# Performance work log

Hardware: AMD Instinct MI355X
Metric: run time of the kernel (lower is better)

Reference implementation:

```python
import jax, jax.numpy as jnp
import numpy as np

NUM_HEADS = 16
HEAD_DIM = 64  # hidden_size (1024) // num_heads


def setup_inputs() -> dict:
    key = jax.random.key(0)
    ks = jax.random.split(key, 8)
    B, S, H = 8, 1024, 1024
    scale = 1.0 / np.sqrt(H)
    return {
        "hidden_states": jax.random.normal(ks[0], (B, S, H), dtype=jnp.float32),
        "attention_mask": jnp.zeros((B, 1, 1, S), dtype=jnp.float32),
        "Wq": jax.random.normal(ks[1], (H, H), dtype=jnp.float32) * scale,
        "bq": jnp.zeros((H,), dtype=jnp.float32),
        "Wk": jax.random.normal(ks[2], (H, H), dtype=jnp.float32) * scale,
        "bk": jnp.zeros((H,), dtype=jnp.float32),
        "Wv": jax.random.normal(ks[3], (H, H), dtype=jnp.float32) * scale,
        "bv": jnp.zeros((H,), dtype=jnp.float32),
    }


def _split_heads(x):
    # [B, S, H] -> [B, nh, S, hd]
    B, S, H = x.shape
    return x.reshape(B, S, NUM_HEADS, HEAD_DIM).transpose(0, 2, 1, 3)


def reference(hidden_states, attention_mask, Wq, bq, Wk, bk, Wv, bv):
    # Q/K/V projections (Keras Dense: y = x @ W + b)
    q = _split_heads(hidden_states @ Wq + bq)  # [B, nh, S, hd]
    k = _split_heads(hidden_states @ Wk + bk)
    v = _split_heads(hidden_states @ Wv + bv)

    # Full QK^T score matrix, scaled, plus additive mask (faithful to source)
    scores = jnp.einsum("bhqd,bhkd->bhqk", q, k) / jnp.sqrt(
        jnp.asarray(HEAD_DIM, dtype=q.dtype)
    )
    scores = scores + attention_mask
    probs = jax.nn.softmax(scores, axis=-1)  # [B, nh, Sq, Sk]

    # Weighted sum of values, merge heads back
    ctx = jnp.einsum("bhqk,bhkd->bhqd", probs, v)
    B, _, S, _ = ctx.shape
    ctx = ctx.transpose(0, 2, 1, 3).reshape(B, S, NUM_HEADS * HEAD_DIM)
    return ctx
```

## Files before the change

### kernel.cpp

```cpp
#include <hip/hip_runtime.h>
#include <hip/hip_bf16.h>


typedef float f4 __attribute__((ext_vector_type(4)));
typedef short s8 __attribute__((ext_vector_type(8)));
typedef short s4 __attribute__((ext_vector_type(4)));

#define NB   8
#define SS   1024
#define HH   1024

#define OFF_XB  0u
#define OFF_WT  16777216u
#define OFF_Q   23068672u
#define OFF_K   39845888u
#define OFF_VT  56623104u

static __device__ __forceinline__ unsigned short f2bf(float x){
    unsigned int u = __float_as_uint(x);
    unsigned int r = (u + 0x7fffu + ((u >> 16) & 1u)) >> 16;
    return (unsigned short)r;
}

__global__ void cvt_x_kernel(const float* __restrict__ in, unsigned short* __restrict__ out){
    int i = blockIdx.x * 256 + threadIdx.x;
    f4 a = ((const f4*)in)[2*i];
    f4 b = ((const f4*)in)[2*i+1];
    s8 r;
    #pragma unroll
    for (int j=0;j<4;j++) r[j]   = (short)f2bf(a[j]);
    #pragma unroll
    for (int j=0;j<4;j++) r[4+j] = (short)f2bf(b[j]);
    ((s8*)out)[i] = r;
}

__global__ void cvt_w_kernel(const float* __restrict__ Wq, const float* __restrict__ Wk,
                             const float* __restrict__ Wv, unsigned short* __restrict__ Wt){
    int t = blockIdx.x;
    int which = t >> 8; t &= 255;
    int k0 = (t >> 4) << 6;
    int n0 = (t & 15) << 6;
    const float* W = which==0 ? Wq : (which==1 ? Wk : Wv);
    __shared__ float Ls[64][65];
    int tid = threadIdx.x;
    #pragma unroll
    for (int i=0;i<4;i++){
        int u = tid + i*256;
        int r = u >> 4, ch = u & 15;
        f4 v = *(const f4*)&W[(size_t)(k0 + r)*HH + n0 + ch*4];
        Ls[r][ch*4+0]=v[0]; Ls[r][ch*4+1]=v[1]; Ls[r][ch*4+2]=v[2]; Ls[r][ch*4+3]=v[3];
    }
    __syncthreads();
    #pragma unroll
    for (int i=0;i<2;i++){
        int u = tid + i*256;
        int nl = u >> 3, kc = u & 7;
        s8 o;
        #pragma unroll
        for (int j=0;j<8;j++) o[j] = (short)f2bf(Ls[kc*8+j][nl]);
        *(s8*)&Wt[(size_t)which*HH*HH + (size_t)(n0+nl)*HH + k0 + kc*8] = o;
    }
}

__global__ __launch_bounds__(256,2) void qkv_gemm_kernel(
    const unsigned short* __restrict__ Xb, const unsigned short* __restrict__ Wt,
    const float* __restrict__ bq, const float* __restrict__ bk, const float* __restrict__ bv,
    unsigned short* __restrict__ Qb, unsigned short* __restrict__ Kb, unsigned short* __restrict__ Vt)
{
    int bid = blockIdx.x;
    bid = (bid & 7)*192 + (bid >> 3);
    int ntile = bid % 24, mtile = bid / 24;
    int which = ntile >> 3;
    int n0 = (ntile & 7) << 7;
    int m0 = mtile << 7;

    __shared__ unsigned short As[128*64];
    __shared__ unsigned short Bs[128*64];

    int tid  = threadIdx.x;
    int lane = tid & 63, wid = tid >> 6;
    int g = lane >> 4, c = lane & 15;
    int wm = wid >> 1, wn = wid & 1;

    const unsigned short* Wp = Wt + (size_t)which * (HH*HH);

    f4 acc[4][4] = {};

    for (int k0 = 0; k0 < HH; k0 += 64) {
        __syncthreads();
        #pragma unroll
        for (int i = 0; i < 4; i++) {
            int base = i*256 + wid*64;
            int t = base + lane;
            int row = t >> 3, sl = t & 7;
            int sg = sl ^ (row & 7);
            __builtin_amdgcn_global_load_lds(
                (const __attribute__((address_space(1))) void*)(Xb + (size_t)(m0+row)*HH + k0 + sg*8),
                (__attribute__((address_space(3))) void*)(As + base*8), 16, 0, 0);
        }
        #pragma unroll
        for (int i = 0; i < 4; i++) {
            int base = i*256 + wid*64;
            int t = base + lane;
            int row = t >> 3, sl = t & 7;
            int sg = sl ^ (row & 7);
            __builtin_amdgcn_global_load_lds(
                (const __attribute__((address_space(1))) void*)(Wp + (size_t)(n0+row)*HH + k0 + sg*8),
                (__attribute__((address_space(3))) void*)(Bs + base*8), 16, 0, 0);
        }
        __syncthreads();
        #pragma unroll
        for (int ks = 0; ks < 2; ks++) {
            s8 af[4], bf[4];
            #pragma unroll
            for (int mi=0;mi<4;mi++){
                int row = wm*64 + mi*16 + c;
                int slot = (ks*4 + g) ^ (row & 7);
                af[mi] = *(const s8*)&As[row*64 + slot*8];
            }
            #pragma unroll
            for (int ni=0;ni<4;ni++){
                int row = wn*64 + ni*16 + c;
                int slot = (ks*4 + g) ^ (row & 7);
                bf[ni] = *(const s8*)&Bs[row*64 + slot*8];
            }
            #pragma unroll
            for (int mi=0;mi<4;mi++)
                #pragma unroll
                for (int ni=0;ni<4;ni++)
                    acc[mi][ni] = __builtin_amdgcn_mfma_f32_16x16x32_bf16(af[mi], bf[ni], acc[mi][ni], 0,0,0);
        }
    }

    if (which < 2) {
        float scl = (which==0) ? 0.125f : 1.0f;
        const float* bias = which==0?bq:bk;
        unsigned short* Out = which==0?Qb:Kb;
        #pragma unroll
        for (int ni=0;ni<4;ni++){
            int col = n0 + wn*64 + ni*16 + c;
            float bb = bias[col];
            #pragma unroll
            for (int mi=0;mi<4;mi++){
                #pragma unroll
                for (int r=0;r<4;r++){
                    int row = m0 + wm*64 + mi*16 + 4*g + r;
                    Out[(size_t)row*HH + col] = f2bf((acc[mi][ni][r] + bb)*scl);
                }
            }
        }
    } else {
        #pragma unroll
        for (int ni=0;ni<4;ni++){
            int col = n0 + wn*64 + ni*16 + c;
            int hh = col >> 6, dd = col & 63;
            float bb = bv[col];
            #pragma unroll
            for (int mi=0;mi<4;mi++){
                int mbase = m0 + wm*64 + mi*16 + 4*g;
                int bb_i = mbase >> 10, s = mbase & 1023;
                s4 vv;
                #pragma unroll
                for (int r=0;r<4;r++) vv[r] = (short)f2bf(acc[mi][ni][r] + bb);
                *(s4*)&Vt[((size_t)((bb_i*16 + hh)*64 + dd))*SS + s] = vv;
            }
        }
    }
}

__global__ __launch_bounds__(256,4) void attn_kernel(
    const unsigned short* __restrict__ Qb, const unsigned short* __restrict__ Kb,
    const unsigned short* __restrict__ Vt, const float* __restrict__ mask,
    float* __restrict__ out)
{
    int bh = blockIdx.y;
    int b = bh >> 4, h = bh & 15;
    int q0 = blockIdx.x << 6;
    int tid = threadIdx.x;
    int w = tid >> 6, lane = tid & 63, g = lane >> 4, c = lane & 15;

    __shared__ unsigned short Ks[2][64*64];
    __shared__ unsigned short pl[4][16][72];

    int qrow = q0 + w*16 + c;
    const unsigned short* Qp = Qb + (size_t)(b*SS + qrow)*HH + h*64;
    s8 qf0 = *(const s8*)(Qp + 8*g);
    s8 qf1 = *(const s8*)(Qp + 32 + 8*g);

    const unsigned short* Kp = Kb + (size_t)(b*SS)*HH + h*64;
    const unsigned short* Vp = Vt + (size_t)(bh*64)*SS;
    const float* mrow = mask + b*SS;

    int lin0 = w*64 + lane;
    int row0 = lin0 >> 3, ch0 = lin0 & 7;
    int src0 = row0*HH + ((ch0 ^ (row0 & 7)) << 3);
    int lin1 = 256 + w*64 + lane;
    int row1 = lin1 >> 3, ch1 = lin1 & 7;
    int src1 = row1*HH + ((ch1 ^ (row1 & 7)) << 3);

    float lsum = 0.f;
    f4 ctx[4] = {};

    __builtin_amdgcn_global_load_lds(
        (const __attribute__((address_space(1))) void*)(Kp + src0),
        (__attribute__((address_space(3))) void*)(&Ks[0][0] + lin0*8), 16, 0, 0);
    __builtin_amdgcn_global_load_lds(
        (const __attribute__((address_space(1))) void*)(Kp + src1),
        (__attribute__((address_space(3))) void*)(&Ks[0][0] + lin1*8), 16, 0, 0);
    __syncthreads();

    for (int t = 0; t < 16; ++t) {
        int cur = t & 1;
        int kv0 = t << 6;
        int nk  = ((t+1) & 15) << 6;
        __builtin_amdgcn_global_load_lds(
            (const __attribute__((address_space(1))) void*)(Kp + (size_t)nk*HH + src0),
            (__attribute__((address_space(3))) void*)(&Ks[cur^1][0] + lin0*8), 16, 0, 0);
        __builtin_amdgcn_global_load_lds(
            (const __attribute__((address_space(1))) void*)(Kp + (size_t)nk*HH + src1),
            (__attribute__((address_space(3))) void*)(&Ks[cur^1][0] + lin1*8), 16, 0, 0);

        f4 mk[4];
        #pragma unroll
        for (int mt=0;mt<4;mt++) mk[mt] = *(const f4*)&mrow[kv0 + mt*16 + 4*g];

        s8 vf0[4];
        #pragma unroll
        for (int dt=0;dt<4;dt++)
            vf0[dt] = *(const s8*)(Vp + (size_t)(dt*16 + c)*SS + kv0 + 8*g);

        s8 kf[8];
        #pragma unroll
        for (int mt=0;mt<4;mt++){
            int rb = (mt*16 + c) << 6;
            int s0 = (g ^ (c & 7)) << 3;
            int s1 = ((4 + g) ^ (c & 7)) << 3;
            kf[2*mt]   = *(const s8*)&Ks[cur][rb + s0];
            kf[2*mt+1] = *(const s8*)&Ks[cur][rb + s1];
        }

        f4 sacc[4] = {};
        __builtin_amdgcn_s_setprio(1);
        #pragma unroll
        for (int mt=0;mt<4;mt++){
            sacc[mt] = __builtin_amdgcn_mfma_f32_16x16x32_bf16(kf[2*mt],   qf0, sacc[mt],0,0,0);
            sacc[mt] = __builtin_amdgcn_mfma_f32_16x16x32_bf16(kf[2*mt+1], qf1, sacc[mt],0,0,0);
        }
        __builtin_amdgcn_s_setprio(0);

        #pragma unroll
        for (int mt=0;mt<4;mt++){
            s4 pk;
            #pragma unroll
            for (int r=0;r<4;r++){
                float pe = __expf(sacc[mt][r] + mk[mt][r]);
                lsum += pe;
                pk[r] = (short)f2bf(pe);
            }
            *(s4*)&pl[w][c][mt*16 + 4*g] = pk;
        }

        s8 vf1[4];
        #pragma unroll
        for (int dt=0;dt<4;dt++)
            vf1[dt] = *(const s8*)(Vp + (size_t)(dt*16 + c)*SS + kv0 + 32 + 8*g);

        s8 pf0 = *(const s8*)&pl[w][c][8*g];
        __builtin_amdgcn_s_setprio(1);
        #pragma unroll
        for (int dt=0;dt<4;dt++)
            ctx[dt] = __builtin_amdgcn_mfma_f32_16x16x32_bf16(vf0[dt], pf0, ctx[dt],0,0,0);
        __builtin_amdgcn_s_setprio(0);
        s8 pf1 = *(const s8*)&pl[w][c][32 + 8*g];
        __builtin_amdgcn_s_setprio(1);
        #pragma unroll
        for (int dt=0;dt<4;dt++)
            ctx[dt] = __builtin_amdgcn_mfma_f32_16x16x32_bf16(vf1[dt], pf1, ctx[dt],0,0,0);
        __builtin_amdgcn_s_setprio(0);

        __syncthreads();
    }

    lsum += __shfl_xor(lsum, 16);
    lsum += __shfl_xor(lsum, 32);
    float inv = 1.0f / lsum;
    #pragma unroll
    for (int dt=0;dt<4;dt++){
        f4 v = ctx[dt]*inv;
        *(f4*)&out[(size_t)(b*SS + qrow)*HH + h*64 + dt*16 + 4*g] = v;
    }
}

extern "C" void kernel_launch(void* const* d_in, const int* in_sizes, int n_in,
                              void* d_out, int out_size, void* d_ws, size_t ws_size,
                              hipStream_t stream)
{
    const float* hs   = (const float*)d_in[0];
    const float* mask = (const float*)d_in[1];
    const float* Wq   = (const float*)d_in[2];
    const float* bq   = (const float*)d_in[3];
    const float* Wk   = (const float*)d_in[4];
    const float* bk   = (const float*)d_in[5];
    const float* Wv   = (const float*)d_in[6];
    const float* bv   = (const float*)d_in[7];
    char* ws = (char*)d_ws;
    unsigned short* Xb = (unsigned short*)(ws + OFF_XB);
    unsigned short* Wt = (unsigned short*)(ws + OFF_WT);
    unsigned short* Qb = (unsigned short*)(ws + OFF_Q);
    unsigned short* Kb = (unsigned short*)(ws + OFF_K);
    unsigned short* Vt = (unsigned short*)(ws + OFF_VT);
    float* out = (float*)d_out;

    cvt_x_kernel<<<4096, 256, 0, stream>>>(hs, Xb);
    cvt_w_kernel<<<768, 256, 0, stream>>>(Wq, Wk, Wv, Wt);
    qkv_gemm_kernel<<<1536, 256, 0, stream>>>(Xb, Wt, bq, bk, bv, Qb, Kb, Vt);
    attn_kernel<<<dim3(16,128), 256, 0, stream>>>(Qb, Kb, Vt, mask, out);
}
```

Measured before the change: 295.3 us.

## Switch attention to 32x32x16 MFMA with register-resident probabilities via lane shuffles

The attention kernel now runs two waves per block, each owning 32 query rows. It uses 32x32x16 bf16 MFMA instead of 16x16x32 for both the QK^T and PV products. The probability tile no longer round-trips through LDS: exponentials are packed with v_cvt_pk_bf16_f32 and exchanged between half-waves with shuffles to form the B operand directly. This removes LDS writes and reads and a conversion sequence, at the cost of more registers per wave and fewer waves per block, which lowers occupancy and latency hiding.

```diff
diff --git a/kernel.cpp b/kernel.cpp
--- a/kernel.cpp
+++ b/kernel.cpp
@@ -2,9 +2,11 @@
 #include <hip/hip_bf16.h>
 
 
-typedef float f4 __attribute__((ext_vector_type(4)));
-typedef short s8 __attribute__((ext_vector_type(8)));
-typedef short s4 __attribute__((ext_vector_type(4)));
+typedef float f4  __attribute__((ext_vector_type(4)));
+typedef float f16v __attribute__((ext_vector_type(16)));
+typedef short s8  __attribute__((ext_vector_type(8)));
+typedef short s4  __attribute__((ext_vector_type(4)));
+typedef int   i4  __attribute__((ext_vector_type(4)));
 
 #define NB   8
 #define SS   1024
@@ -20,6 +22,12 @@
     unsigned int u = __float_as_uint(x);
     unsigned int r = (u + 0x7fffu + ((u >> 16) & 1u)) >> 16;
     return (unsigned short)r;
+}
+
+static __device__ __forceinline__ int cvtpk(float lo, float hi){
+    int w;
+    asm("v_cvt_pk_bf16_f32 %0, %1, %2" : "=v"(w) : "v"(lo), "v"(hi));
+    return w;
 }
 
 __global__ void cvt_x_kernel(const float* __restrict__ in, unsigned short* __restrict__ out){
@@ -168,7 +176,7 @@
     }
 }
 
-__global__ __launch_bounds__(256,4) void attn_kernel(
+__global__ __launch_bounds__(128,2) void attn_kernel(
     const unsigned short* __restrict__ Qb, const unsigned short* __restrict__ Kb,
     const unsigned short* __restrict__ Vt, const float* __restrict__ mask,
     float* __restrict__ out)
@@ -177,117 +185,125 @@
     int b = bh >> 4, h = bh & 15;
     int q0 = blockIdx.x << 6;
     int tid = threadIdx.x;
-    int w = tid >> 6, lane = tid & 63, g = lane >> 4, c = lane & 15;
+    int w = tid >> 6, lane = tid & 63;
+    int lq = lane & 31, hb = lane >> 5;
 
     __shared__ unsigned short Ks[2][64*64];
-    __shared__ unsigned short pl[4][16][72];
-
-    int qrow = q0 + w*16 + c;
+
+    int qrow = q0 + w*32 + lq;
     const unsigned short* Qp = Qb + (size_t)(b*SS + qrow)*HH + h*64;
-    s8 qf0 = *(const s8*)(Qp + 8*g);
-    s8 qf1 = *(const s8*)(Qp + 32 + 8*g);
+    s8 qf[4];
+    #pragma unroll
+    for (int t=0;t<4;t++) qf[t] = *(const s8*)(Qp + 16*t + 8*hb);
 
     const unsigned short* Kp = Kb + (size_t)(b*SS)*HH + h*64;
     const unsigned short* Vp = Vt + (size_t)(bh*64)*SS;
     const float* mrow = mask + b*SS;
 
-    int lin0 = w*64 + lane;
-    int row0 = lin0 >> 3, ch0 = lin0 & 7;
-    int src0 = row0*HH + ((ch0 ^ (row0 & 7)) << 3);
-    int lin1 = 256 + w*64 + lane;
-    int row1 = lin1 >> 3, ch1 = lin1 & 7;
-    int src1 = row1*HH + ((ch1 ^ (row1 & 7)) << 3);
+    int lin[4], src[4];
+    #pragma unroll
+    for (int i=0;i<4;i++){
+        lin[i] = i*128 + tid;
+        int row = lin[i] >> 3, ch = lin[i] & 7;
+        src[i] = row*HH + ((ch ^ (row & 7)) << 3);
+    }
 
     float lsum = 0.f;
-    f4 ctx[4] = {};
-
-    __builtin_amdgcn_global_load_lds(
-        (const __attribute__((address_space(1))) void*)(Kp + src0),
-        (__attribute__((address_space(3))) void*)(&Ks[0][0] + lin0*8), 16, 0, 0);
-    __builtin_amdgcn_global_load_lds(
-        (const __attribute__((address_space(1))) void*)(Kp + src1),
-        (__attribute__((address_space(3))) void*)(&Ks[0][0] + lin1*8), 16, 0, 0);
+    f16v ctxA = {}, ctxB = {};
+
+    #pragma unroll
+    for (int i=0;i<4;i++)
+        __builtin_amdgcn_global_load_lds(
+            (const __attribute__((address_space(1))) void*)(Kp + src[i]),
+            (__attribute__((address_space(3))) void*)(&Ks[0][0] + lin[i]*8), 16, 0, 0);
     __syncthreads();
 
     for (int t = 0; t < 16; ++t) {
         int cur = t & 1;
         int kv0 = t << 6;
         int nk  = ((t+1) & 15) << 6;
-        __builtin_amdgcn_global_load_lds(
-            (const __attribute__((address_space(1))) void*)(Kp + (size_t)nk*HH + src0),
-            (__attribute__((address_space(3))) void*)(&Ks[cur^1][0] + lin0*8), 16, 0, 0);
-        __builtin_amdgcn_global_load_lds(
-            (const __attribute__((address_space(1))) void*)(Kp + (size_t)nk*HH + src1),
-            (__attribute__((address_space(3))) void*)(&Ks[cur^1][0] + lin1*8), 16, 0, 0);
-
-        f4 mk[4];
-        #pragma unroll
-        for (int mt=0;mt<4;mt++) mk[mt] = *(const f4*)&mrow[kv0 + mt*16 + 4*g];
-
-        s8 vf0[4];
-        #pragma unroll
-        for (int dt=0;dt<4;dt++)
-            vf0[dt] = *(const s8*)(Vp + (size_t)(dt*16 + c)*SS + kv0 + 8*g);
-
-        s8 kf[8];
-        #pragma unroll
-        for (int mt=0;mt<4;mt++){
-            int rb = (mt*16 + c) << 6;
-            int s0 = (g ^ (c & 7)) << 3;
-            int s1 = ((4 + g) ^ (c & 7)) << 3;
-            kf[2*mt]   = *(const s8*)&Ks[cur][rb + s0];
-            kf[2*mt+1] = *(const s8*)&Ks[cur][rb + s1];
-        }
-
-        f4 sacc[4] = {};
+        #pragma unroll
+        for (int i=0;i<4;i++)
+            __builtin_amdgcn_global_load_lds(
+                (const __attribute__((address_space(1))) void*)(Kp + (size_t)nk*HH + src[i]),
+                (__attribute__((address_space(3))) void*)(&Ks[cur^1][0] + lin[i]*8), 16, 0, 0);
+
+        s8 vf[2][4];
+        #pragma unroll
+        for (int dt=0;dt<2;dt++)
+            #pragma unroll
+            for (int s=0;s<4;s++)
+                vf[dt][s] = *(const s8*)(Vp + (size_t)(dt*32 + lq)*SS + kv0 + 16*s + 8*hb);
+        f4 mA[4], mB[4];
+        #pragma unroll
+        for (int tp=0;tp<4;tp++){
+            mA[tp] = *(const f4*)&mrow[kv0 + 8*tp + 4*hb];
+            mB[tp] = *(const f4*)&mrow[kv0 + 32 + 8*tp + 4*hb];
+        }
+
+        s8 kA[4], kB[4];
+        #pragma unroll
+        for (int tt=0;tt<4;tt++){
+            int sl = (2*tt + hb) ^ (lq & 7);
+            kA[tt] = *(const s8*)&Ks[cur][lq*64 + sl*8];
+            kB[tt] = *(const s8*)&Ks[cur][(32+lq)*64 + sl*8];
+        }
+
+        f16v sA = {}, sB = {};
         __builtin_amdgcn_s_setprio(1);
         #pragma unroll
-        for (int mt=0;mt<4;mt++){
-            sacc[mt] = __builtin_amdgcn_mfma_f32_16x16x32_bf16(kf[2*mt],   qf0, sacc[mt],0,0,0);
-            sacc[mt] = __builtin_amdgcn_mfma_f32_16x16x32_bf16(kf[2*mt+1], qf1, sacc[mt],0,0,0);
+        for (int tt=0;tt<4;tt++){
+            sA = __builtin_amdgcn_mfma_f32_32x32x16_bf16(kA[tt], qf[tt], sA, 0,0,0);
+            sB = __builtin_amdgcn_mfma_f32_32x32x16_bf16(kB[tt], qf[tt], sB, 0,0,0);
         }
         __builtin_amdgcn_s_setprio(0);
 
-        #pragma unroll
-        for (int mt=0;mt<4;mt++){
-            s4 pk;
-            #pragma unroll
-            for (int r=0;r<4;r++){
-                float pe = __expf(sacc[mt][r] + mk[mt][r]);
-                lsum += pe;
-                pk[r] = (short)f2bf(pe);
-            }
-            *(s4*)&pl[w][c][mt*16 + 4*g] = pk;
-        }
-
-        s8 vf1[4];
-        #pragma unroll
-        for (int dt=0;dt<4;dt++)
-            vf1[dt] = *(const s8*)(Vp + (size_t)(dt*16 + c)*SS + kv0 + 32 + 8*g);
-
-        s8 pf0 = *(const s8*)&pl[w][c][8*g];
+        float eA[16], eB[16];
+        #pragma unroll
+        for (int r=0;r<16;r++){
+            eA[r] = __expf(sA[r] + mA[r>>2][r&3]);
+            eB[r] = __expf(sB[r] + mB[r>>2][r&3]);
+            lsum += eA[r] + eB[r];
+        }
+
+        int wA0=cvtpk(eA[0],eA[1]),  wA1=cvtpk(eA[2],eA[3]),  wA2=cvtpk(eA[4],eA[5]),  wA3=cvtpk(eA[6],eA[7]);
+        int wA4=cvtpk(eA[8],eA[9]),  wA5=cvtpk(eA[10],eA[11]),wA6=cvtpk(eA[12],eA[13]),wA7=cvtpk(eA[14],eA[15]);
+        int wB0=cvtpk(eB[0],eB[1]),  wB1=cvtpk(eB[2],eB[3]),  wB2=cvtpk(eB[4],eB[5]),  wB3=cvtpk(eB[6],eB[7]);
+        int wB4=cvtpk(eB[8],eB[9]),  wB5=cvtpk(eB[10],eB[11]),wB6=cvtpk(eB[12],eB[13]),wB7=cvtpk(eB[14],eB[15]);
+        int xA0=__shfl_xor(wA0,32), xA1=__shfl_xor(wA1,32), xA2=__shfl_xor(wA2,32), xA3=__shfl_xor(wA3,32);
+        int xA4=__shfl_xor(wA4,32), xA5=__shfl_xor(wA5,32), xA6=__shfl_xor(wA6,32), xA7=__shfl_xor(wA7,32);
+        int xB0=__shfl_xor(wB0,32), xB1=__shfl_xor(wB1,32), xB2=__shfl_xor(wB2,32), xB3=__shfl_xor(wB3,32);
+        int xB4=__shfl_xor(wB4,32), xB5=__shfl_xor(wB5,32), xB6=__shfl_xor(wB6,32), xB7=__shfl_xor(wB7,32);
+        bool H = (hb != 0);
+        i4 p0 = { H?xA2:wA0, H?xA3:wA1, H?wA2:xA0, H?wA3:xA1 };
+        i4 p1 = { H?xA6:wA4, H?xA7:wA5, H?wA6:xA4, H?wA7:xA5 };
+        i4 p2 = { H?xB2:wB0, H?xB3:wB1, H?wB2:xB0, H?wB3:xB1 };
+        i4 p3 = { H?xB6:wB4, H?xB7:wB5, H?wB6:xB4, H?wB7:xB5 };
+        s8 pf0 = *(s8*)&p0, pf1 = *(s8*)&p1, pf2 = *(s8*)&p2, pf3 = *(s8*)&p3;
+
         __builtin_amdgcn_s_setprio(1);
-        #pragma unroll
-        for (int dt=0;dt<4;dt++)
-            ctx[dt] = __builtin_amdgcn_mfma_f32_16x16x32_bf16(vf0[dt], pf0, ctx[dt],0,0,0);
+        ctxA = __builtin_amdgcn_mfma_f32_32x32x16_bf16(vf[0][0], pf0, ctxA, 0,0,0);
+        ctxB = __builtin_amdgcn_mfma_f32_32x32x16_bf16(vf[1][0], pf0, ctxB, 0,0,0);
+        ctxA = __builtin_amdgcn_mfma_f32_32x32x16_bf16(vf[0][1], pf1, ctxA, 0,0,0);
+        ctxB = __builtin_amdgcn_mfma_f32_32x32x16_bf16(vf[1][1], pf1, ctxB, 0,0,0);
+        ctxA = __builtin_amdgcn_mfma_f32_32x32x16_bf16(vf[0][2], pf2, ctxA, 0,0,0);
+        ctxB = __builtin_amdgcn_mfma_f32_32x32x16_bf16(vf[1][2], pf2, ctxB, 0,0,0);
+        ctxA = __builtin_amdgcn_mfma_f32_32x32x16_bf16(vf[0][3], pf3, ctxA, 0,0,0);
+        ctxB = __builtin_amdgcn_mfma_f32_32x32x16_bf16(vf[1][3], pf3, ctxB, 0,0,0);
         __builtin_amdgcn_s_setprio(0);
-        s8 pf1 = *(const s8*)&pl[w][c][32 + 8*g];
-        __builtin_amdgcn_s_setprio(1);
-        #pragma unroll
-        for (int dt=0;dt<4;dt++)
-            ctx[dt] = __builtin_amdgcn_mfma_f32_16x16x32_bf16(vf1[dt], pf1, ctx[dt],0,0,0);
-        __builtin_amdgcn_s_setprio(0);
 
         __syncthreads();
     }
 
-    lsum += __shfl_xor(lsum, 16);
     lsum += __shfl_xor(lsum, 32);
     float inv = 1.0f / lsum;
-    #pragma unroll
-    for (int dt=0;dt<4;dt++){
-        f4 v = ctx[dt]*inv;
-        *(f4*)&out[(size_t)(b*SS + qrow)*HH + h*64 + dt*16 + 4*g] = v;
+    float* orow = out + (size_t)(b*SS + qrow)*HH + h*64;
+    #pragma unroll
+    for (int tp=0;tp<4;tp++){
+        f4 va = { ctxA[4*tp]*inv, ctxA[4*tp+1]*inv, ctxA[4*tp+2]*inv, ctxA[4*tp+3]*inv };
+        *(f4*)&orow[8*tp + 4*hb] = va;
+        f4 vb = { ctxB[4*tp]*inv, ctxB[4*tp+1]*inv, ctxB[4*tp+2]*inv, ctxB[4*tp+3]*inv };
+        *(f4*)&orow[32 + 8*tp + 4*hb] = vb;
     }
 }
 
@@ -314,5 +330,5 @@
     cvt_x_kernel<<<4096, 256, 0, stream>>>(hs, Xb);
     cvt_w_kernel<<<768, 256, 0, stream>>>(Wq, Wk, Wv, Wt);
     qkv_gemm_kernel<<<1536, 256, 0, stream>>>(Xb, Wt, bq, bk, bv, Qb, Kb, Vt);
-    attn_kernel<<<dim3(16,128), 256, 0, stream>>>(Qb, Kb, Vt, mask, out);
-}
+    attn_kernel<<<dim3(16,128), 128, 0, stream>>>(Qb, Kb, Vt, mask, out);
+}
```

New measurement: 270.5 us. 8.4% less time.
